# Performance work log

Hardware: AMD Instinct MI355X
Metric: run time of the kernel (lower is better)

The kernel has to match this reference:

```python
import jax, jax.numpy as jnp
import numpy as np

B, D, F, N = 16, 8, 2, 512
E = D + F


def setup_inputs() -> dict:
    key = jax.random.key(0)
    ks = jax.random.split(key, 8)
    obs_mean = jax.random.normal(ks[0], (B, D), jnp.float32)
    action_mean = jax.random.normal(ks[1], (B, F), jnp.float32)
    # joint PSD input covariance over x_tilde = [x, u], then slice blocks
    A = 0.1 * jax.random.normal(ks[2], (B, E, E), jnp.float32)
    J = A @ jnp.swapaxes(A, -1, -2) / E + 0.01 * jnp.eye(E, dtype=jnp.float32)
    obs_var = J[:, :D, :D]
    action_var = J[:, D:, D:]
    cross_cov = J[:, :D, D:]
    X_train = jax.random.normal(ks[3], (N, E), jnp.float32)
    ell = jax.random.uniform(ks[4], (D, E), jnp.float32, 0.7, 1.5)
    alpha_sq = jax.random.uniform(ks[5], (D,), jnp.float32, 0.5, 1.5)
    sigma_sq_eps = 0.01 * jnp.ones((D,), jnp.float32)
    y = 0.1 * jax.random.normal(ks[6], (D, N), jnp.float32)

    def per_dim(ell_a, a2, s2, y_a):
        Xs = X_train / ell_a
        sq = jnp.sum((Xs[:, None, :] - Xs[None, :, :]) ** 2, axis=-1)
        Kn = a2 * jnp.exp(-0.5 * sq) + (s2 + 1e-6) * jnp.eye(N, dtype=jnp.float32)
        invK = jnp.linalg.inv(Kn)
        return invK, invK @ y_a

    inv_K, beta = jax.vmap(per_dim)(ell, alpha_sq, sigma_sq_eps, y)
    return {
        "obs_mean": obs_mean, "obs_var": obs_var,
        "action_mean": action_mean, "action_var": action_var,
        "cross_cov": cross_cov,
        "X_train": X_train, "ell": ell, "alpha_sq": alpha_sq,
        "sigma_sq_eps": sigma_sq_eps, "beta": beta, "inv_K": inv_K,
    }


def reference(obs_mean, obs_var, action_mean, action_var, cross_cov,
              X_train, ell, alpha_sq, sigma_sq_eps, beta, inv_K):
    """PILCO moment matching (Deisenroth & Rasmussen 2011, Eqs. 10-23).

    One SE-ARD GP per output dim a predicts the residual Delta_a; a Gaussian
    joint belief N(mu, Sigma) over x_tilde = [x, u] is propagated analytically.
    Returns (mu_next [B,D], Sigma_next [B,D,D]).
    """
    f32 = jnp.float32
    mu = jnp.concatenate([obs_mean, action_mean], axis=-1)              # [B,E]
    top = jnp.concatenate([obs_var, cross_cov], axis=-1)                # [B,D,E]
    bot = jnp.concatenate([jnp.swapaxes(cross_cov, -1, -2), action_var], axis=-1)
    Sigma = jnp.concatenate([top, bot], axis=-2)                        # [B,E,E]

    nu = X_train[None, :, :] - mu[:, None, :]                           # [B,N,E]
    ell2 = ell ** 2                                                     # [D,E]
    iLam = 1.0 / ell2                                                   # [D,E]
    Lam = jax.vmap(jnp.diag)(ell2)                                      # [D,E,E]

    # ---- predictive mean (Eqs. 10-12): q_ai = a2 |Sigma iLam + I|^{-1/2}
    #      exp(-0.5 nu_i^T (Sigma+Lam)^{-1} nu_i)
    Amat = Sigma[:, None, :, :] + Lam[None, :, :, :]                    # [B,D,E,E]
    Ainv = jnp.linalg.inv(Amat)
    logdetA = jnp.linalg.slogdet(Amat)[1]                               # [B,D]
    logdetLam = jnp.sum(jnp.log(ell2), axis=-1)                         # [D]
    quad = jnp.einsum('bne,bdef,bnf->bdn', nu, Ainv, nu)
    q = alpha_sq[None, :, None] * jnp.exp(
        0.5 * (logdetLam[None, :] - logdetA)[..., None] - 0.5 * quad)   # [B,D,N]
    mu_delta = jnp.einsum('dn,bdn->bd', beta, q)                        # [B,D]

    # ---- input-output covariance Cov[x_tilde, Delta_a]
    w = jnp.einsum('dn,bdn,bne->bde', beta, q, nu)                      # [B,D,E]
    V = jnp.einsum('bef,bdfg,bdg->bde', Sigma, Ainv, w)                 # [B,D,E]

    # ---- predictive covariance (Eqs. 20-23)
    logk = jnp.log(alpha_sq)[None, :, None] - 0.5 * jnp.einsum(
        'bne,de->bdn', nu ** 2, iLam)                                   # [B,D,N]
    P = nu[:, None, :, :] * iLam[None, :, None, :]                      # [B,D,N,E]
    eyeE = jnp.eye(E, dtype=f32)

    rows, traces = [], []
    for a in range(D):  # loop over obs dims (structurally distinct pairs)
        iLsum = iLam[a][None, :] + iLam                                 # [D,E]
        R = Sigma[:, None, :, :] * iLsum[None, :, None, :] + eyeE       # [B,D,E,E]
        S = jnp.linalg.solve(R, jnp.broadcast_to(Sigma[:, None], R.shape))
        logdetR = jnp.linalg.slogdet(R)[1]                              # [B,D]
        Pa = P[:, a]                                                    # [B,N,E]
        d_a = jnp.einsum('bie,bdef,bif->bdi', Pa, S, Pa)                # [B,D,N]
        d_b = jnp.einsum('bdje,bdef,bdjf->bdj', P, S, P)                # [B,D,N]
        m = jnp.einsum('bie,bdef,bdjf->bdij', Pa, S, P)                 # [B,D,N,N]
        c_a = logk[:, a][:, None, :] + 0.5 * d_a
        c_b = logk + 0.5 * d_b
        Q = jnp.exp(c_a[..., :, None] + m + c_b[..., None, :]
                    - 0.5 * logdetR[..., None, None])                   # [B,D,N,N]
        rows.append(jnp.einsum('i,bdij,dj->bd', beta[a], Q, beta))
        traces.append(jnp.einsum('ij,bij->b', inv_K[a], Q[:, a]))

    EDD = jnp.stack(rows, axis=1)                                       # [B,D,D]
    tr = jnp.stack(traces, axis=1)                                      # [B,D]
    Sigma_delta = EDD - mu_delta[:, :, None] * mu_delta[:, None, :]
    Sigma_delta = 0.5 * (Sigma_delta + jnp.swapaxes(Sigma_delta, -1, -2))
    diag_corr = alpha_sq[None, :] - tr + sigma_sq_eps[None, :]          # [B,D]
    Sigma_delta = Sigma_delta + jax.vmap(jnp.diag)(diag_corr)

    # ---- next-state moments: x_next = x + Delta
    C_xd = jnp.swapaxes(V[..., :D], 1, 2)                               # [B,Dx,Dd]
    mu_next = obs_mean + mu_delta
    Sigma_next = obs_var + Sigma_delta + C_xd + jnp.swapaxes(C_xd, -1, -2)
    return mu_next, Sigma_next
```

## Files before the change

kernel.cpp:

```cpp
#include <hip/hip_runtime.h>
#include <math.h>

#define B 16
#define D 8
#define FDIM 2
#define N 512
#define E 10
#define NP36 36
#define GJW (2*E)
#define NT 4
#define TIL 128
#define NQ (NP36*B*NT)
#define NPREP (NP36*B + B*D)
#define LOG2E 1.44269504088896340736f
#define KA 12

#define OFF_MUD  0
#define OFF_V    128
#define OFF_EDDP 1408
#define OFF_TRP  3712
#define OFF_W    4224
#define OFF_CA   61824
#define OFF_CB   356736

typedef _Float16 f16x4 __attribute__((ext_vector_type(4)));
typedef float f32x4 __attribute__((ext_vector_type(4)));

__device__ __forceinline__ float exp2_hw(float x) {
  float r;
  __asm__ __volatile__("v_exp_f32 %0, %1" : "=v"(r) : "v"(x));
  return r;
}

__device__ __forceinline__ void decode_pair(int p36, int* pa, int* pd) {
  int a = 0, rem = p36;
  while (rem >= D - a) { rem -= (D - a); a++; }
  *pa = a; *pd = a + rem;
}

__device__ __forceinline__ float wave_reduce(float v) {
#pragma unroll
  for (int off = 32; off > 0; off >>= 1) v += __shfl_down(v, off);
  return v;
}

__device__ __forceinline__ void wsync() {
  __asm__ __volatile__("" ::: "memory");
  __builtin_amdgcn_wave_barrier();
  __asm__ __volatile__("" ::: "memory");
}

__device__ __forceinline__ float gj_wave(float (*M)[GJW], int lane) {
  float pivs[E];
#pragma unroll
  for (int k = 0; k < E; k++) {
    wsync();
    int pr = k;
    float best = fabsf(M[k][k]);
#pragma unroll
    for (int r = 1; r < E; r++) {
      if (r > k) {
        float v = fabsf(M[r][k]);
        if (v > best) { best = v; pr = r; }
      }
    }
    pivs[k] = M[pr][k];
    wsync();
    float tk = 0.f, pw = 0.f;
    if (lane < GJW) {
      float piv = M[pr][k];
      pw = M[pr][lane] / piv;
      tk = M[k][lane];
    }
    wsync();
    if (lane < GJW) {
      M[pr][lane] = tk;
      M[k][lane]  = pw;
    }
    wsync();
    float cf[4], pv[4], cur[4];
    int rr[4], cc[4];
#pragma unroll
    for (int t = 0; t < 4; t++) {
      int idx = lane + t * 64;
      if (idx < E * GJW) {
        int r = idx / GJW, c = idx - r * GJW;
        rr[t] = r; cc[t] = c;
        cf[t]  = M[r][k];
        pv[t]  = M[k][c];
        cur[t] = M[r][c];
      } else {
        rr[t] = k; cc[t] = 0; cf[t] = 0.f; pv[t] = 0.f; cur[t] = 0.f;
      }
    }
    wsync();
#pragma unroll
    for (int t = 0; t < 4; t++) {
      int idx = lane + t * 64;
      if (idx < E * GJW && rr[t] != k) {
        M[rr[t]][cc[t]] = fmaf(-cf[t], pv[t], cur[t]);
      }
    }
  }
  wsync();
  float ld = 0.f;
#pragma unroll
  for (int k = 0; k < E; k++) ld += logf(fabsf(pivs[k]));
  return ld;
}

__global__ __launch_bounds__(256) void k_prep(
    const float* __restrict__ obs_mean, const float* __restrict__ obs_var,
    const float* __restrict__ action_mean, const float* __restrict__ action_var,
    const float* __restrict__ cross_cov, const float* __restrict__ X,
    const float* __restrict__ ell, const float* __restrict__ alpha_sq,
    const float* __restrict__ beta, float* __restrict__ ws) {
  __shared__ float M[E][GJW];
  __shared__ float s_logdet;
  __shared__ float sMu[E], sSig[E * E], siLa[E], siLd[E];
  __shared__ float wred[4][11];
  __shared__ float wsh[E];

  int tid = threadIdx.x;
  int bx = blockIdx.x;

  if (bx >= NP36 * B) {
    int bd = bx - NP36 * B;
    int b = bd / D, d = bd % D;
    if (tid < E) {
      sMu[tid] = (tid < D) ? obs_mean[b * D + tid] : action_mean[b * FDIM + tid - D];
    }
    for (int idx = tid; idx < E * E; idx += 256) {
      int e = idx / E, f = idx % E;
      float v;
      if (e < D && f < D)      v = obs_var[(b * D + e) * D + f];
      else if (e < D)          v = cross_cov[(b * D + e) * FDIM + (f - D)];
      else if (f < D)          v = cross_cov[(b * D + f) * FDIM + (e - D)];
      else                     v = action_var[(b * FDIM + (e - D)) * FDIM + (f - D)];
      sSig[idx] = v;
    }
    __syncthreads();
    for (int idx = tid; idx < E * GJW; idx += 256) {
      int r = idx / GJW, c = idx % GJW;
      float v;
      if (c < E) {
        v = sSig[r * E + c];
        if (r == c) { float l = ell[d * E + r]; v += l * l; }
      } else {
        v = (c - E == r) ? 1.0f : 0.0f;
      }
      M[r][c] = v;
    }
    __syncthreads();
    if (tid < 64) {
      float ld = gj_wave(M, tid);
      if (tid == 0) s_logdet = ld;
    }
    __syncthreads();
    float lda = s_logdet;
    float a2 = alpha_sq[d];
    float logdetLam = 0.0f;
#pragma unroll
    for (int e = 0; e < E; e++) { float l = ell[d * E + e]; logdetLam += logf(l * l); }
    float c0 = 0.5f * (logdetLam - lda);
    float acc_mu = 0.0f, acc_w[E];
#pragma unroll
    for (int e = 0; e < E; e++) acc_w[e] = 0.0f;
    for (int n = tid; n < N; n += 256) {
      float x[E];
#pragma unroll
      for (int e = 0; e < E; e++) x[e] = X[n * E + e] - sMu[e];
      float quad = 0.0f;
#pragma unroll
      for (int e = 0; e < E; e++) {
        float te = 0.0f;
#pragma unroll
        for (int f = 0; f < E; f++) te += M[e][E + f] * x[f];
        quad += x[e] * te;
      }
      float qval = a2 * __expf(c0 - 0.5f * quad);
      float bq = beta[d * N + n] * qval;
      acc_mu += bq;
#pragma unroll
      for (int e = 0; e < E; e++) acc_w[e] += bq * x[e];
    }
    int wid = tid >> 6, lane = tid & 63;
    float r = wave_reduce(acc_mu);
    if (lane == 0) wred[wid][0] = r;
#pragma unroll
    for (int e = 0; e < E; e++) {
      r = wave_reduce(acc_w[e]);
      if (lane == 0) wred[wid][e + 1] = r;
    }
    __syncthreads();
    if (tid < 11) {
      float s = wred[0][tid] + wred[1][tid] + wred[2][tid] + wred[3][tid];
      if (tid == 0) ws[OFF_MUD + b * D + d] = s;
      else wsh[tid - 1] = s;
    }
    __syncthreads();
    if (tid == 0) {
      float u[E];
#pragma unroll
      for (int f = 0; f < E; f++) {
        float s = 0.0f;
#pragma unroll
        for (int g = 0; g < E; g++) s += M[f][E + g] * wsh[g];
        u[f] = s;
      }
#pragma unroll
      for (int e = 0; e < E; e++) {
        float s = 0.0f;
#pragma unroll
        for (int f = 0; f < E; f++) s += sSig[e * E + f] * u[f];
        ws[OFF_V + (b * D + d) * E + e] = s;
      }
    }
    return;
  }

  int p36 = bx / B, b = bx % B;
  int a, d;
  decode_pair(p36, &a, &d);
  int pb = p36 * B + b;
  if (tid < E) {
    sMu[tid] = (tid < D) ? obs_mean[b * D + tid] : action_mean[b * FDIM + tid - D];
    float la = ell[a * E + tid]; siLa[tid] = 1.0f / (la * la);
    float ld = ell[d * E + tid]; siLd[tid] = 1.0f / (ld * ld);
  }
  for (int idx = tid; idx < E * E; idx += 256) {
    int e = idx / E, f = idx % E;
    float v;
    if (e < D && f < D)      v = obs_var[(b * D + e) * D + f];
    else if (e < D)          v = cross_cov[(b * D + e) * FDIM + (f - D)];
    else if (f < D)          v = cross_cov[(b * D + f) * FDIM + (e - D)];
    else                     v = action_var[(b * FDIM + (e - D)) * FDIM + (f - D)];
    sSig[idx] = v;
  }
  __syncthreads();
  for (int idx = tid; idx < E * GJW; idx += 256) {
    int r = idx / GJW, c = idx % GJW;
    float v;
    if (c < E) v = sSig[r * E + c] * (siLa[c] + siLd[c]) + ((r == c) ? 1.0f : 0.0f);
    else       v = sSig[r * E + (c - E)];
    M[r][c] = v;
  }
  __syncthreads();
  if (tid < 64) {
    float ld = gj_wave(M, tid);
    if (tid == 0) s_logdet = ld;
  }
  __syncthreads();
  float ldr = s_logdet;
  float lga = logf(alpha_sq[a]);
  float lgd = logf(alpha_sq[d]);
  for (int idx = tid; idx < E * E; idx += 256) {
    int e = idx / E, f = idx % E;
    ws[OFF_W + pb * (E * E) + idx] = LOG2E * M[e][E + f] * siLa[e] * siLd[f];
  }
  for (int n = tid; n < N; n += 256) {
    float x[E], pa[E], pd[E];
    float s2a = 0.0f, s2b = 0.0f;
#pragma unroll
    for (int e = 0; e < E; e++) {
      float xe = X[n * E + e] - sMu[e];
      x[e] = xe;
      pa[e] = xe * siLa[e];
      pd[e] = xe * siLd[e];
      s2a += xe * pa[e];
      s2b += xe * pd[e];
    }
    float da = 0.0f, db = 0.0f;
#pragma unroll
    for (int e = 0; e < E; e++) {
      float ta = 0.0f, td = 0.0f;
#pragma unroll
      for (int f = 0; f < E; f++) {
        float s = M[e][E + f];
        ta += s * pa[f];
        td += s * pd[f];
      }
      da += pa[e] * ta;
      db += pd[e] * td;
    }
    ws[OFF_CA + pb * N + n] = LOG2E * (lga - 0.5f * s2a + 0.5f * da - 0.5f * ldr);
    ws[OFF_CB + pb * N + n] = LOG2E * (lgd - 0.5f * s2b + 0.5f * db);
  }
}

__global__ __launch_bounds__(256) void k_q(
    const float* __restrict__ obs_mean, const float* __restrict__ action_mean,
    const float* __restrict__ X, const float* __restrict__ beta,
    const float* __restrict__ invK, float* __restrict__ ws) {
  __shared__ __attribute__((aligned(16))) _Float16 snh[N * KA];
  __shared__ __attribute__((aligned(16))) _Float16 snl[N * KA];
  __shared__ __attribute__((aligned(16))) _Float16 sTh[TIL * KA + 8];
  __shared__ __attribute__((aligned(16))) _Float16 sTl[TIL * KA + 8];
  __shared__ float sW[E * E];
  __shared__ float sMu[E];
  __shared__ __attribute__((aligned(16))) float sba[TIL];
  __shared__ float redw[8];

  int tid = threadIdx.x;
  int bx = blockIdx.x;
  int tile = bx & (NT - 1);
  int rest = bx >> 2;
  int b = rest & (B - 1);
  int p36 = rest >> 4;
  int a, d;
  decode_pair(p36, &a, &d);
  int pb = p36 * B + b;
  bool diag = (a == d);
  int i0 = tile * TIL;

  if (tid < E) sMu[tid] = (tid < D) ? obs_mean[b * D + tid] : action_mean[b * FDIM + tid - D];
  if (tid < E * E) sW[tid] = ws[OFF_W + pb * (E * E) + tid];
  if (tid < TIL) sba[tid] = beta[a * N + i0 + tid];
  if (tid < 8) { sTh[TIL * KA + tid] = (_Float16)0.f; sTl[TIL * KA + tid] = (_Float16)0.f; }
  __syncthreads();

  for (int jj = tid; jj < N; jj += 256) {
    float v[KA];
#pragma unroll
    for (int e = 0; e < E; e++) v[e] = X[jj * E + e] - sMu[e];
    v[10] = 1.0f;
    v[11] = ws[OFF_CB + (size_t)pb * N + jj];
#pragma unroll
    for (int k = 0; k < KA; k++) {
      _Float16 h = (_Float16)v[k];
      snh[jj * KA + k] = h;
      snl[jj * KA + k] = (_Float16)(v[k] - (float)h);
    }
  }

  {
    int il = tid >> 1;
    int k0 = (tid & 1) * 6;
    float nu[E];
#pragma unroll
    for (int e = 0; e < E; e++) nu[e] = X[(i0 + il) * E + e] - sMu[e];
#pragma unroll
    for (int kk = 0; kk < 6; kk++) {
      int k = k0 + kk;
      float v;
      if (k < E) {
        v = 0.f;
#pragma unroll
        for (int e = 0; e < E; e++) v = fmaf(nu[e], sW[e * E + k], v);
      } else if (k == E) {
        v = ws[OFF_CA + (size_t)pb * N + i0 + il];
      } else {
        v = 1.0f;
      }
      _Float16 h = (_Float16)v;
      sTh[il * KA + k] = h;
      sTl[il * KA + k] = (_Float16)(v - (float)h);
    }
  }
  __syncthreads();

  int lane = tid & 63;
  int w = tid >> 6;
  int c = lane & 15;
  int kg = lane >> 4;
  bool kval = (kg < 3);
  int koff = kg * 4;
  float accR = 0.f;
  float accT0 = 0.f, accT1 = 0.f, accT2 = 0.f, accT3 = 0.f;
  const float* invKa = invK + (size_t)a * N * N;
  const f32x4 zero4 = {0.f, 0.f, 0.f, 0.f};

  for (int jt8 = 0; jt8 < 8; jt8++) {
    int jt = (w << 3) + jt8;
    int j = (jt << 4) + c;
    f16x4 Bh = {(_Float16)0.f, (_Float16)0.f, (_Float16)0.f, (_Float16)0.f};
    f16x4 Bl = {(_Float16)0.f, (_Float16)0.f, (_Float16)0.f, (_Float16)0.f};
    if (kval) {
      Bh = *(const f16x4*)&snh[j * KA + koff];
      Bl = *(const f16x4*)&snl[j * KA + koff];
    }
    float bd = beta[d * N + j];
    const float* kvrow = invKa + (size_t)j * N + i0 + koff;
#pragma unroll
    for (int it = 0; it < 8; it++) {
      const f16x4 Ah = *(const f16x4*)&sTh[(it * 16 + c) * KA + koff];
      const f16x4 Al = *(const f16x4*)&sTl[(it * 16 + c) * KA + koff];
      f32x4 m = __builtin_amdgcn_mfma_f32_16x16x16f16(Ah, Bh, zero4, 0, 0, 0);
      m = __builtin_amdgcn_mfma_f32_16x16x16f16(Ah, Bl, m, 0, 0, 0);
      m = __builtin_amdgcn_mfma_f32_16x16x16f16(Al, Bh, m, 0, 0, 0);
      float q0 = exp2_hw(m[0]);
      float q1 = exp2_hw(m[1]);
      float q2 = exp2_hw(m[2]);
      float q3 = exp2_hw(m[3]);
      f32x4 ba = *(const f32x4*)&sba[it * 16 + koff];
      float t = ba[0] * q0;
      t = fmaf(ba[1], q1, t);
      t = fmaf(ba[2], q2, t);
      t = fmaf(ba[3], q3, t);
      accR = fmaf(bd, t, accR);
      if (diag) {
        f32x4 r = *(const f32x4*)(kvrow + it * 16);
        accT0 = fmaf(r[0], q0, accT0);
        accT1 = fmaf(r[1], q1, accT1);
        accT2 = fmaf(r[2], q2, accT2);
        accT3 = fmaf(r[3], q3, accT3);
      }
    }
  }

  {
    float rr = wave_reduce(accR);
    int wid = tid >> 6, ln = tid & 63;
    if (ln == 0) redw[wid] = rr;
    if (diag) {
      float rt = wave_reduce((accT0 + accT1) + (accT2 + accT3));
      if (ln == 0) redw[4 + wid] = rt;
    }
    __syncthreads();
    if (tid == 0) {
      ws[OFF_EDDP + (p36 * B + b) * NT + tile] = redw[0] + redw[1] + redw[2] + redw[3];
      if (diag)
        ws[OFF_TRP + (a * B + b) * NT + tile] = redw[4] + redw[5] + redw[6] + redw[7];
    }
  }
}

__global__ __launch_bounds__(64) void k_final(
    const float* __restrict__ obs_mean, const float* __restrict__ obs_var,
    const float* __restrict__ alpha_sq, const float* __restrict__ sigma_sq_eps,
    const float* __restrict__ ws, float* __restrict__ out) {
  int b = blockIdx.x;
  int tid = threadIdx.x;
  const float* mud = ws + OFF_MUD + b * D;
  if (tid < D) out[b * D + tid] = obs_mean[b * D + tid] + mud[tid];
  if (tid < D * D) {
    int i = tid / D, j = tid % D;
    int a = i < j ? i : j;
    int dd = i < j ? j : i;
    int p36 = a * D - a * (a - 1) / 2 + (dd - a);
    float edd = 0.0f;
#pragma unroll
    for (int tt = 0; tt < NT; tt++) edd += ws[OFF_EDDP + (p36 * B + b) * NT + tt];
    float sd = edd - mud[i] * mud[j];
    if (i == j) {
      float tr = 0.0f;
#pragma unroll
      for (int tt = 0; tt < NT; tt++) tr += ws[OFF_TRP + (i * B + b) * NT + tt];
      sd += alpha_sq[i] - tr + sigma_sq_eps[i];
    }
    const float* V = ws + OFF_V;
    float cxd = V[(b * D + j) * E + i];
    float cdx = V[(b * D + i) * E + j];
    out[B * D + b * D * D + tid] = obs_var[b * D * D + tid] + sd + cxd + cdx;
  }
}

extern "C" void kernel_launch(void* const* d_in, const int* in_sizes, int n_in,
                              void* d_out, int out_size, void* d_ws, size_t ws_size,
                              hipStream_t stream) {
  const float* obs_mean     = (const float*)d_in[0];
  const float* obs_var      = (const float*)d_in[1];
  const float* action_mean  = (const float*)d_in[2];
  const float* action_var   = (const float*)d_in[3];
  const float* cross_cov    = (const float*)d_in[4];
  const float* X_train      = (const float*)d_in[5];
  const float* ell          = (const float*)d_in[6];
  const float* alpha_sq     = (const float*)d_in[7];
  const float* sigma_sq_eps = (const float*)d_in[8];
  const float* beta         = (const float*)d_in[9];
  const float* inv_K        = (const float*)d_in[10];
  float* out = (float*)d_out;
  float* ws = (float*)d_ws;

  k_prep<<<NPREP, 256, 0, stream>>>(obs_mean, obs_var, action_mean, action_var,
                                    cross_cov, X_train, ell, alpha_sq, beta, ws);
  k_q<<<NQ, 256, 0, stream>>>(obs_mean, action_mean, X_train, beta, inv_K, ws);
  k_final<<<B, 64, 0, stream>>>(obs_mean, obs_var, alpha_sq, sigma_sq_eps, ws, out);
}
```

Baseline: 154.6 us.

## Fuse prep and Q kernels into one, recomputing per-pair setup per tile

Merges the per-pair preparation kernel (Gauss-Jordan solve, W matrix, c_a/c_b log terms) into the MFMA Q kernel, so W, c_a and c_b stay in shared memory and are never written to and re-read from the workspace. The i-tile grows from 128 to 256 rows, halving tiles per pair so the duplicated GJ solve and c_b computation is repeated twice per pair instead of four times. This removes a kernel launch and global round-trip. In exchange it costs redundant setup work per tile, fewer blocks in the grid, and a larger shared-memory footprint that may lower occupancy.

```diff
diff --git a/kernel.cpp b/kernel.cpp
--- a/kernel.cpp
+++ b/kernel.cpp
@@ -8,20 +8,17 @@
 #define E 10
 #define NP36 36
 #define GJW (2*E)
-#define NT 4
-#define TIL 128
-#define NQ (NP36*B*NT)
-#define NPREP (NP36*B + B*D)
+#define NT 2
+#define TIL 256
+#define KA 12
+#define NPAIRB (NP36*B*NT)
+#define NMAIN (NPAIRB + B*D)
 #define LOG2E 1.44269504088896340736f
-#define KA 12
 
 #define OFF_MUD  0
 #define OFF_V    128
 #define OFF_EDDP 1408
-#define OFF_TRP  3712
-#define OFF_W    4224
-#define OFF_CA   61824
-#define OFF_CB   356736
+#define OFF_TRP  2560
 
 typedef _Float16 f16x4 __attribute__((ext_vector_type(4)));
 typedef float f32x4 __attribute__((ext_vector_type(4)));
@@ -109,23 +106,32 @@
   return ld;
 }
 
-__global__ __launch_bounds__(256) void k_prep(
+__global__ __launch_bounds__(256) void k_main(
     const float* __restrict__ obs_mean, const float* __restrict__ obs_var,
     const float* __restrict__ action_mean, const float* __restrict__ action_var,
     const float* __restrict__ cross_cov, const float* __restrict__ X,
     const float* __restrict__ ell, const float* __restrict__ alpha_sq,
-    const float* __restrict__ beta, float* __restrict__ ws) {
+    const float* __restrict__ beta, const float* __restrict__ invK,
+    float* __restrict__ ws) {
+  __shared__ __attribute__((aligned(16))) _Float16 snh[N * KA];
+  __shared__ __attribute__((aligned(16))) _Float16 snl[N * KA];
+  __shared__ __attribute__((aligned(16))) _Float16 sTh[TIL * KA + 8];
+  __shared__ __attribute__((aligned(16))) _Float16 sTl[TIL * KA + 8];
   __shared__ float M[E][GJW];
+  __shared__ float sSig[E * E];
+  __shared__ float sW[E * E];
+  __shared__ float sMu[E], siLa[E], siLd[E];
+  __shared__ __attribute__((aligned(16))) float sba[TIL];
+  __shared__ float redw[8];
   __shared__ float s_logdet;
-  __shared__ float sMu[E], sSig[E * E], siLa[E], siLd[E];
   __shared__ float wred[4][11];
   __shared__ float wsh[E];
 
   int tid = threadIdx.x;
   int bx = blockIdx.x;
 
-  if (bx >= NP36 * B) {
-    int bd = bx - NP36 * B;
+  if (bx >= NPAIRB) {
+    int bd = bx - NPAIRB;
     int b = bd / D, d = bd % D;
     if (tid < E) {
       sMu[tid] = (tid < D) ? obs_mean[b * D + tid] : action_mean[b * FDIM + tid - D];
@@ -219,10 +225,15 @@
     return;
   }
 
-  int p36 = bx / B, b = bx % B;
+  int tile = bx & (NT - 1);
+  int rest = bx >> 1;
+  int b = rest & (B - 1);
+  int p36 = rest >> 4;
   int a, d;
   decode_pair(p36, &a, &d);
-  int pb = p36 * B + b;
+  bool diag = (a == d);
+  int i0 = tile * TIL;
+
   if (tid < E) {
     sMu[tid] = (tid < D) ? obs_mean[b * D + tid] : action_mean[b * FDIM + tid - D];
     float la = ell[a * E + tid]; siLa[tid] = 1.0f / (la * la);
@@ -254,77 +265,35 @@
   float ldr = s_logdet;
   float lga = logf(alpha_sq[a]);
   float lgd = logf(alpha_sq[d]);
-  for (int idx = tid; idx < E * E; idx += 256) {
-    int e = idx / E, f = idx % E;
-    ws[OFF_W + pb * (E * E) + idx] = LOG2E * M[e][E + f] * siLa[e] * siLd[f];
-  }
-  for (int n = tid; n < N; n += 256) {
-    float x[E], pa[E], pd[E];
-    float s2a = 0.0f, s2b = 0.0f;
+  if (tid < E * E) {
+    int e = tid / E, f = tid % E;
+    sW[tid] = LOG2E * M[e][E + f] * siLa[e] * siLd[f];
+  }
+
+  for (int jj = tid; jj < N; jj += 256) {
+    float x[E], pd_[E];
+    float s2b = 0.0f;
 #pragma unroll
     for (int e = 0; e < E; e++) {
-      float xe = X[n * E + e] - sMu[e];
+      float xe = X[jj * E + e] - sMu[e];
       x[e] = xe;
-      pa[e] = xe * siLa[e];
-      pd[e] = xe * siLd[e];
-      s2a += xe * pa[e];
-      s2b += xe * pd[e];
-    }
-    float da = 0.0f, db = 0.0f;
+      pd_[e] = xe * siLd[e];
+      s2b += xe * pd_[e];
+    }
+    float db = 0.0f;
 #pragma unroll
     for (int e = 0; e < E; e++) {
-      float ta = 0.0f, td = 0.0f;
-#pragma unroll
-      for (int f = 0; f < E; f++) {
-        float s = M[e][E + f];
-        ta += s * pa[f];
-        td += s * pd[f];
-      }
-      da += pa[e] * ta;
-      db += pd[e] * td;
-    }
-    ws[OFF_CA + pb * N + n] = LOG2E * (lga - 0.5f * s2a + 0.5f * da - 0.5f * ldr);
-    ws[OFF_CB + pb * N + n] = LOG2E * (lgd - 0.5f * s2b + 0.5f * db);
-  }
-}
-
-__global__ __launch_bounds__(256) void k_q(
-    const float* __restrict__ obs_mean, const float* __restrict__ action_mean,
-    const float* __restrict__ X, const float* __restrict__ beta,
-    const float* __restrict__ invK, float* __restrict__ ws) {
-  __shared__ __attribute__((aligned(16))) _Float16 snh[N * KA];
-  __shared__ __attribute__((aligned(16))) _Float16 snl[N * KA];
-  __shared__ __attribute__((aligned(16))) _Float16 sTh[TIL * KA + 8];
-  __shared__ __attribute__((aligned(16))) _Float16 sTl[TIL * KA + 8];
-  __shared__ float sW[E * E];
-  __shared__ float sMu[E];
-  __shared__ __attribute__((aligned(16))) float sba[TIL];
-  __shared__ float redw[8];
-
-  int tid = threadIdx.x;
-  int bx = blockIdx.x;
-  int tile = bx & (NT - 1);
-  int rest = bx >> 2;
-  int b = rest & (B - 1);
-  int p36 = rest >> 4;
-  int a, d;
-  decode_pair(p36, &a, &d);
-  int pb = p36 * B + b;
-  bool diag = (a == d);
-  int i0 = tile * TIL;
-
-  if (tid < E) sMu[tid] = (tid < D) ? obs_mean[b * D + tid] : action_mean[b * FDIM + tid - D];
-  if (tid < E * E) sW[tid] = ws[OFF_W + pb * (E * E) + tid];
-  if (tid < TIL) sba[tid] = beta[a * N + i0 + tid];
-  if (tid < 8) { sTh[TIL * KA + tid] = (_Float16)0.f; sTl[TIL * KA + tid] = (_Float16)0.f; }
-  __syncthreads();
-
-  for (int jj = tid; jj < N; jj += 256) {
+      float td = 0.0f;
+#pragma unroll
+      for (int f = 0; f < E; f++) td += M[e][E + f] * pd_[f];
+      db += pd_[e] * td;
+    }
+    float cb = LOG2E * (lgd - 0.5f * s2b + 0.5f * db);
     float v[KA];
 #pragma unroll
-    for (int e = 0; e < E; e++) v[e] = X[jj * E + e] - sMu[e];
+    for (int e = 0; e < E; e++) v[e] = x[e];
     v[10] = 1.0f;
-    v[11] = ws[OFF_CB + (size_t)pb * N + jj];
+    v[11] = cb;
 #pragma unroll
     for (int k = 0; k < KA; k++) {
       _Float16 h = (_Float16)v[k];
@@ -332,31 +301,47 @@
       snl[jj * KA + k] = (_Float16)(v[k] - (float)h);
     }
   }
+  __syncthreads();
 
   {
-    int il = tid >> 1;
-    int k0 = (tid & 1) * 6;
-    float nu[E];
-#pragma unroll
-    for (int e = 0; e < E; e++) nu[e] = X[(i0 + il) * E + e] - sMu[e];
-#pragma unroll
-    for (int kk = 0; kk < 6; kk++) {
-      int k = k0 + kk;
-      float v;
-      if (k < E) {
-        v = 0.f;
-#pragma unroll
-        for (int e = 0; e < E; e++) v = fmaf(nu[e], sW[e * E + k], v);
-      } else if (k == E) {
-        v = ws[OFF_CA + (size_t)pb * N + i0 + il];
-      } else {
-        v = 1.0f;
-      }
-      _Float16 h = (_Float16)v;
+    int il = tid;
+    float x[E], pa_[E];
+    float s2a = 0.0f;
+#pragma unroll
+    for (int e = 0; e < E; e++) {
+      float xe = X[(i0 + il) * E + e] - sMu[e];
+      x[e] = xe;
+      pa_[e] = xe * siLa[e];
+      s2a += xe * pa_[e];
+    }
+    float da = 0.0f;
+#pragma unroll
+    for (int e = 0; e < E; e++) {
+      float ta = 0.0f;
+#pragma unroll
+      for (int f = 0; f < E; f++) ta += M[e][E + f] * pa_[f];
+      da += pa_[e] * ta;
+    }
+    float ca = LOG2E * (lga - 0.5f * s2a + 0.5f * da - 0.5f * ldr);
+    float t[KA];
+#pragma unroll
+    for (int f = 0; f < E; f++) {
+      float s = 0.0f;
+#pragma unroll
+      for (int e = 0; e < E; e++) s = fmaf(x[e], sW[e * E + f], s);
+      t[f] = s;
+    }
+    t[10] = ca;
+    t[11] = 1.0f;
+#pragma unroll
+    for (int k = 0; k < KA; k++) {
+      _Float16 h = (_Float16)t[k];
       sTh[il * KA + k] = h;
-      sTl[il * KA + k] = (_Float16)(v - (float)h);
-    }
-  }
+      sTl[il * KA + k] = (_Float16)(t[k] - (float)h);
+    }
+    sba[il] = beta[a * N + i0 + il];
+  }
+  if (tid < 8) { sTh[TIL * KA + tid] = (_Float16)0.f; sTl[TIL * KA + tid] = (_Float16)0.f; }
   __syncthreads();
 
   int lane = tid & 63;
@@ -382,7 +367,7 @@
     float bd = beta[d * N + j];
     const float* kvrow = invKa + (size_t)j * N + i0 + koff;
 #pragma unroll
-    for (int it = 0; it < 8; it++) {
+    for (int it = 0; it < 16; it++) {
       const f16x4 Ah = *(const f16x4*)&sTh[(it * 16 + c) * KA + koff];
       const f16x4 Al = *(const f16x4*)&sTl[(it * 16 + c) * KA + koff];
       f32x4 m = __builtin_amdgcn_mfma_f32_16x16x16f16(Ah, Bh, zero4, 0, 0, 0);
@@ -472,8 +457,8 @@
   float* out = (float*)d_out;
   float* ws = (float*)d_ws;
 
-  k_prep<<<NPREP, 256, 0, stream>>>(obs_mean, obs_var, action_mean, action_var,
-                                    cross_cov, X_train, ell, alpha_sq, beta, ws);
-  k_q<<<NQ, 256, 0, stream>>>(obs_mean, action_mean, X_train, beta, inv_K, ws);
+  k_main<<<NMAIN, 256, 0, stream>>>(obs_mean, obs_var, action_mean, action_var,
+                                    cross_cov, X_train, ell, alpha_sq, beta,
+                                    inv_K, ws);
   k_final<<<B, 64, 0, stream>>>(obs_mean, obs_var, alpha_sq, sigma_sq_eps, ws, out);
 }
```

Result: slower. 179.7 us (+16.3%).

## Map one prep system per wavefront instead of per block in k_prep

Applied to the files above, without the earlier changes.

k_prep now packs four independent systems into each 256-thread block, one per wavefront, with per-wave shared-memory slices and wave-level sync in place of block-wide barriers. Previously three of four waves sat idle during the Gauss-Jordan solve. The inverse matrix is also copied into registers for the per-point quadratic forms, and the cross-wave reduction step is removed. Each wave now handles all 512 training points alone, so per-wave work grows and the register arrays raise register pressure.

```diff
diff --git a/kernel.cpp b/kernel.cpp
--- a/kernel.cpp
+++ b/kernel.cpp
@@ -11,7 +11,8 @@
 #define NT 4
 #define TIL 128
 #define NQ (NP36*B*NT)
-#define NPREP (NP36*B + B*D)
+#define NSYS (NP36*B + B*D)
+#define NPREPB (NSYS/4)
 #define LOG2E 1.44269504088896340736f
 #define KA 12
 
@@ -115,49 +116,48 @@
     const float* __restrict__ cross_cov, const float* __restrict__ X,
     const float* __restrict__ ell, const float* __restrict__ alpha_sq,
     const float* __restrict__ beta, float* __restrict__ ws) {
-  __shared__ float M[E][GJW];
-  __shared__ float s_logdet;
-  __shared__ float sMu[E], sSig[E * E], siLa[E], siLd[E];
-  __shared__ float wred[4][11];
-  __shared__ float wsh[E];
+  __shared__ float M[4][E][GJW];
+  __shared__ float sSig[4][E * E];
+  __shared__ float sMu[4][E], siLa[4][E], siLd[4][E];
 
   int tid = threadIdx.x;
-  int bx = blockIdx.x;
-
-  if (bx >= NP36 * B) {
-    int bd = bx - NP36 * B;
-    int b = bd / D, d = bd % D;
-    if (tid < E) {
-      sMu[tid] = (tid < D) ? obs_mean[b * D + tid] : action_mean[b * FDIM + tid - D];
-    }
-    for (int idx = tid; idx < E * E; idx += 256) {
+  int wid = tid >> 6, lane = tid & 63;
+  int sid = blockIdx.x * 4 + wid;
+
+  if (sid >= NP36 * B) {
+    int bd = sid - NP36 * B;
+    int b = bd >> 3, d = bd & 7;
+    if (lane < E) {
+      sMu[wid][lane] = (lane < D) ? obs_mean[b * D + lane]
+                                  : action_mean[b * FDIM + lane - D];
+    }
+    for (int idx = lane; idx < E * E; idx += 64) {
       int e = idx / E, f = idx % E;
       float v;
       if (e < D && f < D)      v = obs_var[(b * D + e) * D + f];
       else if (e < D)          v = cross_cov[(b * D + e) * FDIM + (f - D)];
       else if (f < D)          v = cross_cov[(b * D + f) * FDIM + (e - D)];
       else                     v = action_var[(b * FDIM + (e - D)) * FDIM + (f - D)];
-      sSig[idx] = v;
-    }
-    __syncthreads();
-    for (int idx = tid; idx < E * GJW; idx += 256) {
+      sSig[wid][idx] = v;
+    }
+    wsync();
+    for (int idx = lane; idx < E * GJW; idx += 64) {
       int r = idx / GJW, c = idx % GJW;
       float v;
       if (c < E) {
-        v = sSig[r * E + c];
+        v = sSig[wid][r * E + c];
         if (r == c) { float l = ell[d * E + r]; v += l * l; }
       } else {
         v = (c - E == r) ? 1.0f : 0.0f;
       }
-      M[r][c] = v;
-    }
-    __syncthreads();
-    if (tid < 64) {
-      float ld = gj_wave(M, tid);
-      if (tid == 0) s_logdet = ld;
-    }
-    __syncthreads();
-    float lda = s_logdet;
+      M[wid][r][c] = v;
+    }
+    float lda = gj_wave(M[wid], lane);
+    float Av[E][E];
+#pragma unroll
+    for (int e = 0; e < E; e++)
+#pragma unroll
+      for (int f = 0; f < E; f++) Av[e][f] = M[wid][e][E + f];
     float a2 = alpha_sq[d];
     float logdetLam = 0.0f;
 #pragma unroll
@@ -166,16 +166,18 @@
     float acc_mu = 0.0f, acc_w[E];
 #pragma unroll
     for (int e = 0; e < E; e++) acc_w[e] = 0.0f;
-    for (int n = tid; n < N; n += 256) {
+#pragma unroll
+    for (int t = 0; t < 8; t++) {
+      int n = lane + t * 64;
       float x[E];
 #pragma unroll
-      for (int e = 0; e < E; e++) x[e] = X[n * E + e] - sMu[e];
+      for (int e = 0; e < E; e++) x[e] = X[n * E + e] - sMu[wid][e];
       float quad = 0.0f;
 #pragma unroll
       for (int e = 0; e < E; e++) {
         float te = 0.0f;
 #pragma unroll
-        for (int f = 0; f < E; f++) te += M[e][E + f] * x[f];
+        for (int f = 0; f < E; f++) te += Av[e][f] * x[f];
         quad += x[e] * te;
       }
       float qval = a2 * __expf(c0 - 0.5f * quad);
@@ -184,91 +186,81 @@
 #pragma unroll
       for (int e = 0; e < E; e++) acc_w[e] += bq * x[e];
     }
-    int wid = tid >> 6, lane = tid & 63;
-    float r = wave_reduce(acc_mu);
-    if (lane == 0) wred[wid][0] = r;
-#pragma unroll
-    for (int e = 0; e < E; e++) {
-      r = wave_reduce(acc_w[e]);
-      if (lane == 0) wred[wid][e + 1] = r;
-    }
-    __syncthreads();
-    if (tid < 11) {
-      float s = wred[0][tid] + wred[1][tid] + wred[2][tid] + wred[3][tid];
-      if (tid == 0) ws[OFF_MUD + b * D + d] = s;
-      else wsh[tid - 1] = s;
-    }
-    __syncthreads();
-    if (tid == 0) {
+    acc_mu = wave_reduce(acc_mu);
+#pragma unroll
+    for (int e = 0; e < E; e++) acc_w[e] = wave_reduce(acc_w[e]);
+    if (lane == 0) {
+      ws[OFF_MUD + b * D + d] = acc_mu;
       float u[E];
 #pragma unroll
       for (int f = 0; f < E; f++) {
         float s = 0.0f;
 #pragma unroll
-        for (int g = 0; g < E; g++) s += M[f][E + g] * wsh[g];
+        for (int g = 0; g < E; g++) s += Av[f][g] * acc_w[g];
         u[f] = s;
       }
 #pragma unroll
       for (int e = 0; e < E; e++) {
         float s = 0.0f;
 #pragma unroll
-        for (int f = 0; f < E; f++) s += sSig[e * E + f] * u[f];
+        for (int f = 0; f < E; f++) s += sSig[wid][e * E + f] * u[f];
         ws[OFF_V + (b * D + d) * E + e] = s;
       }
     }
     return;
   }
 
-  int p36 = bx / B, b = bx % B;
+  int p36 = sid >> 4, b = sid & 15;
   int a, d;
   decode_pair(p36, &a, &d);
   int pb = p36 * B + b;
-  if (tid < E) {
-    sMu[tid] = (tid < D) ? obs_mean[b * D + tid] : action_mean[b * FDIM + tid - D];
-    float la = ell[a * E + tid]; siLa[tid] = 1.0f / (la * la);
-    float ld = ell[d * E + tid]; siLd[tid] = 1.0f / (ld * ld);
-  }
-  for (int idx = tid; idx < E * E; idx += 256) {
+  if (lane < E) {
+    sMu[wid][lane] = (lane < D) ? obs_mean[b * D + lane]
+                                : action_mean[b * FDIM + lane - D];
+    float la = ell[a * E + lane]; siLa[wid][lane] = 1.0f / (la * la);
+    float ld = ell[d * E + lane]; siLd[wid][lane] = 1.0f / (ld * ld);
+  }
+  for (int idx = lane; idx < E * E; idx += 64) {
     int e = idx / E, f = idx % E;
     float v;
     if (e < D && f < D)      v = obs_var[(b * D + e) * D + f];
     else if (e < D)          v = cross_cov[(b * D + e) * FDIM + (f - D)];
     else if (f < D)          v = cross_cov[(b * D + f) * FDIM + (e - D)];
     else                     v = action_var[(b * FDIM + (e - D)) * FDIM + (f - D)];
-    sSig[idx] = v;
-  }
-  __syncthreads();
-  for (int idx = tid; idx < E * GJW; idx += 256) {
+    sSig[wid][idx] = v;
+  }
+  wsync();
+  for (int idx = lane; idx < E * GJW; idx += 64) {
     int r = idx / GJW, c = idx % GJW;
     float v;
-    if (c < E) v = sSig[r * E + c] * (siLa[c] + siLd[c]) + ((r == c) ? 1.0f : 0.0f);
-    else       v = sSig[r * E + (c - E)];
-    M[r][c] = v;
-  }
-  __syncthreads();
-  if (tid < 64) {
-    float ld = gj_wave(M, tid);
-    if (tid == 0) s_logdet = ld;
-  }
-  __syncthreads();
-  float ldr = s_logdet;
+    if (c < E) v = sSig[wid][r * E + c] * (siLa[wid][c] + siLd[wid][c]) + ((r == c) ? 1.0f : 0.0f);
+    else       v = sSig[wid][r * E + (c - E)];
+    M[wid][r][c] = v;
+  }
+  float ldr = gj_wave(M[wid], lane);
+  float Sv[E][E];
+#pragma unroll
+  for (int e = 0; e < E; e++)
+#pragma unroll
+    for (int f = 0; f < E; f++) Sv[e][f] = M[wid][e][E + f];
   float lga = logf(alpha_sq[a]);
   float lgd = logf(alpha_sq[d]);
-  for (int idx = tid; idx < E * E; idx += 256) {
+  for (int idx = lane; idx < E * E; idx += 64) {
     int e = idx / E, f = idx % E;
-    ws[OFF_W + pb * (E * E) + idx] = LOG2E * M[e][E + f] * siLa[e] * siLd[f];
-  }
-  for (int n = tid; n < N; n += 256) {
-    float x[E], pa[E], pd[E];
+    ws[OFF_W + pb * (E * E) + idx] = LOG2E * Sv[e][f] * siLa[wid][e] * siLd[wid][f];
+  }
+#pragma unroll
+  for (int t = 0; t < 8; t++) {
+    int n = lane + t * 64;
+    float pa_[E], pd_[E];
     float s2a = 0.0f, s2b = 0.0f;
 #pragma unroll
     for (int e = 0; e < E; e++) {
-      float xe = X[n * E + e] - sMu[e];
-      x[e] = xe;
-      pa[e] = xe * siLa[e];
-      pd[e] = xe * siLd[e];
-      s2a += xe * pa[e];
-      s2b += xe * pd[e];
+      float xe = X[n * E + e] - sMu[wid][e];
+      pa_[e] = xe * siLa[wid][e];
+      pd_[e] = xe * siLd[wid][e];
+      s2a += xe * pa_[e];
+      s2b += xe * pd_[e];
     }
     float da = 0.0f, db = 0.0f;
 #pragma unroll
@@ -276,12 +268,12 @@
       float ta = 0.0f, td = 0.0f;
 #pragma unroll
       for (int f = 0; f < E; f++) {
-        float s = M[e][E + f];
-        ta += s * pa[f];
-        td += s * pd[f];
-      }
-      da += pa[e] * ta;
-      db += pd[e] * td;
+        float s = Sv[e][f];
+        ta += s * pa_[f];
+        td += s * pd_[f];
+      }
+      da += pa_[e] * ta;
+      db += pd_[e] * td;
     }
     ws[OFF_CA + pb * N + n] = LOG2E * (lga - 0.5f * s2a + 0.5f * da - 0.5f * ldr);
     ws[OFF_CB + pb * N + n] = LOG2E * (lgd - 0.5f * s2b + 0.5f * db);
@@ -472,8 +464,8 @@
   float* out = (float*)d_out;
   float* ws = (float*)d_ws;
 
-  k_prep<<<NPREP, 256, 0, stream>>>(obs_mean, obs_var, action_mean, action_var,
-                                    cross_cov, X_train, ell, alpha_sq, beta, ws);
+  k_prep<<<NPREPB, 256, 0, stream>>>(obs_mean, obs_var, action_mean, action_var,
+                                     cross_cov, X_train, ell, alpha_sq, beta, ws);
   k_q<<<NQ, 256, 0, stream>>>(obs_mean, action_mean, X_train, beta, inv_K, ws);
   k_final<<<B, 64, 0, stream>>>(obs_mean, obs_var, alpha_sq, sigma_sq_eps, ws, out);
 }
```

Result: faster. 150.7 us (-2.5%).
